# Optimization experiments

Hardware: AMD Instinct MI355X
Metric: run time of the kernel (lower is better)

## Reference

```python
import jax, jax.numpy as jnp
import numpy as np

B, T, I, H = 128, 128, 12, 512


def setup_inputs() -> dict:
    key = jax.random.key(0)
    k1, k2, k3, k4 = jax.random.split(key, 4)
    s_ih = 1.0 / np.sqrt(H)
    return {
        "history": jax.random.normal(k1, (B, T, I), dtype=jnp.float32),
        "W_ih": jax.random.uniform(k2, (3 * H, I), dtype=jnp.float32, minval=-s_ih, maxval=s_ih),
        "W_hh": jax.random.uniform(k3, (3 * H, H), dtype=jnp.float32, minval=-s_ih, maxval=s_ih),
        "W_pred": jax.random.uniform(k4, (2, H), dtype=jnp.float32, minval=-s_ih, maxval=s_ih),
    }


def reference(history, W_ih, W_hh, W_pred):
    # GRUCell (bias=False), PyTorch gate order: r, z, n
    def step(h, x_t):
        gi = x_t @ W_ih.T            # [B, 3H]
        gh = h @ W_hh.T              # [B, 3H]
        i_r, i_z, i_n = jnp.split(gi, 3, axis=-1)
        h_r, h_z, h_n = jnp.split(gh, 3, axis=-1)
        r = jax.nn.sigmoid(i_r + h_r)
        z = jax.nn.sigmoid(i_z + h_z)
        n = jnp.tanh(i_n + r * h_n)
        h_new = (1.0 - z) * n + z * h
        logit = h_new @ W_pred.T     # per-step bubble_prediction head
        return h_new, logit

    h0 = jnp.zeros((history.shape[0], W_hh.shape[1]), dtype=history.dtype)
    xs = jnp.swapaxes(history, 0, 1)          # [T, B, I]
    h_last, logits_tbf = jax.lax.scan(step, h0, xs)
    logits = jnp.swapaxes(logits_tbf, 0, 1)   # [B, T, 2]
    return logits, h_last
```

## Files before the change

kernel.cpp:

```cpp
#include <hip/hip_runtime.h>
#include <cstdint>


typedef __attribute__((ext_vector_type(4))) float f32x4;
typedef __attribute__((ext_vector_type(8))) __bf16 bf16x8;

#define NTHREADS 256
#define CG_N 32
#define BB 16
#define HC 16
#define T_STEPS 128
#define I_DIM 12
#define H_DIM 512

#define WS_HX0   0
#define WS_HX1   262144
#define WS_FLAGS 524288

__device__ __forceinline__ float bf16f(unsigned short u){
  return __uint_as_float(((unsigned int)u) << 16);
}
__device__ __forceinline__ void split_bf16(float x, unsigned short &hi, unsigned short &lo){
  unsigned int u = __float_as_uint(x);
  hi = (unsigned short)(u >> 16);
  float r = x - __uint_as_float((u >> 16) << 16);
  unsigned int ru = __float_as_uint(r);
  ru += 0x7fffu + ((ru >> 16) & 1u);
  lo = (unsigned short)(ru >> 16);
}
__device__ __forceinline__ float fsigmoid(float x){ return 1.0f / (1.0f + __expf(-x)); }
__device__ __forceinline__ float ftanh(float x){ return 2.0f / (1.0f + __expf(-2.0f * x)) - 1.0f; }
__device__ __forceinline__ f32x4 MFMA(bf16x8 a, bf16x8 b, f32x4 c){
  return __builtin_amdgcn_mfma_f32_16x16x32_bf16(a, b, c, 0, 0, 0);
}
__device__ __forceinline__ void wait_vm0(){
  asm volatile("s_waitcnt vmcnt(0)" ::: "memory");
}
__device__ __forceinline__ unsigned int hiP(unsigned int x, unsigned int y){
  return (x >> 16) | (y & 0xFFFF0000u);
}
__device__ __forceinline__ unsigned int loP(unsigned int x, unsigned int y){
  return (x & 0xFFFFu) | (y << 16);
}

__device__ __forceinline__ void dev_store_u32(unsigned int* p, unsigned int v){
  asm volatile("global_store_dword %0, %1, off sc1" :: "v"(p), "v"(v) : "memory");
}
__device__ __forceinline__ unsigned int dev_load_u32(const unsigned int* p){
  unsigned int v;
  asm volatile("global_load_dword %0, %1, off sc1\n\ts_waitcnt vmcnt(0)"
               : "=v"(v) : "v"(p) : "memory");
  return v;
}
__device__ __forceinline__ void load_h_row(const unsigned int* p, uint4* pr){
  uint4 v0, v1, v2, v3, v4, v5, v6, v7;
  asm volatile(
    "global_load_dwordx4 %0, %8, off sc1\n\t"
    "global_load_dwordx4 %1, %8, off offset:16 sc1\n\t"
    "global_load_dwordx4 %2, %8, off offset:32 sc1\n\t"
    "global_load_dwordx4 %3, %8, off offset:48 sc1\n\t"
    "global_load_dwordx4 %4, %8, off offset:64 sc1\n\t"
    "global_load_dwordx4 %5, %8, off offset:80 sc1\n\t"
    "global_load_dwordx4 %6, %8, off offset:96 sc1\n\t"
    "global_load_dwordx4 %7, %8, off offset:112 sc1\n\t"
    "s_waitcnt vmcnt(0)"
    : "=&v"(v0), "=&v"(v1), "=&v"(v2), "=&v"(v3),
      "=&v"(v4), "=&v"(v5), "=&v"(v6), "=&v"(v7)
    : "v"(p) : "memory");
  pr[0]=v0; pr[1]=v1; pr[2]=v2; pr[3]=v3; pr[4]=v4; pr[5]=v5; pr[6]=v6; pr[7]=v7;
}

__device__ __forceinline__ void poll_h_row(const unsigned int* p, uint4* pr,
                                           unsigned int want){
  for (;;){
    load_h_row(p, pr);
    unsigned int diff = 0u;
    #pragma unroll
    for (int b = 0; b < 8; ++b)
      diff |= (pr[b].x ^ want) | (pr[b].y ^ want) | (pr[b].z ^ want) | (pr[b].w ^ want);
    if ((diff & 3u) == 0u) break;
  }
  #pragma unroll
  for (int b = 0; b < 8; ++b){
    pr[b].x &= 0xFFFFFFFCu; pr[b].y &= 0xFFFFFFFCu;
    pr[b].z &= 0xFFFFFFFCu; pr[b].w &= 0xFFFFFFFCu;
  }
}

extern "C" __global__ void __launch_bounds__(NTHREADS, 1)
gru_persistent(const float* __restrict__ hist, const float* __restrict__ wih,
               const float* __restrict__ whh, const float* __restrict__ wpred,
               float* __restrict__ out, unsigned char* __restrict__ ws)
{
  __shared__ __align__(16) unsigned short whi_l[3*16*64*8];
  __shared__ __align__(16) unsigned short wlo_l[3*16*64*8];
  __shared__ __align__(16) unsigned short hhi_l[BB*H_DIM];
  __shared__ __align__(16) unsigned short hlo_l[BB*H_DIM];
  __shared__ __align__(16) float part_l[4*3*64*4];
  __shared__ __align__(16) float x_l[BB*I_DIM];
  __shared__ __align__(16) float wih_l[48*I_DIM];
  __shared__ __align__(16) float wpred_l[2*H_DIM];

  const int tid  = threadIdx.x;
  const int bg   = blockIdx.x & 7;
  const int cg   = blockIdx.x >> 3;
  const int wave = tid >> 6;
  const int lane = tid & 63;

  unsigned int* hx[2] = {(unsigned int*)(ws + WS_HX0), (unsigned int*)(ws + WS_HX1)};
  unsigned int* flagsP = (unsigned int*)(ws + WS_FLAGS);

  for (int i = tid; i < 48*I_DIM; i += NTHREADS){
    int j = i / I_DIM, ii = i % I_DIM;
    int R = (j >> 4)*H_DIM + cg*HC + (j & 15);
    wih_l[i] = wih[R*I_DIM + ii];
  }
  if (cg < 4){
    for (int i = tid; i < 2*H_DIM; i += NTHREADS) wpred_l[i] = wpred[i];
  }
  #pragma unroll
  for (int it = 0; it < 24; ++it){
    int f0 = (it*NTHREADS + tid) * 4;
    int j = f0 >> 9, k = f0 & 511;
    int R = (j >> 4)*H_DIM + cg*HC + (j & 15);
    float4 v = *(const float4*)(whh + R*H_DIM + k);
    int nt = j >> 4;
    int ln = (j & 15) | (((k >> 3) & 3) << 4);
    int kt = k >> 5, e = k & 7;
    int base = (((nt*16 + kt)*64) + ln)*8 + e;
    float vv[4] = {v.x, v.y, v.z, v.w};
    unsigned short h4[4], l4[4];
    #pragma unroll
    for (int q = 0; q < 4; ++q) split_bf16(vv[q], h4[q], l4[q]);
    uint2 uh, ul;
    uh.x = (unsigned int)h4[0] | ((unsigned int)h4[1] << 16);
    uh.y = (unsigned int)h4[2] | ((unsigned int)h4[3] << 16);
    ul.x = (unsigned int)l4[0] | ((unsigned int)l4[1] << 16);
    ul.y = (unsigned int)l4[2] | ((unsigned int)l4[3] << 16);
    *(uint2*)((char*)whi_l + base*2) = uh;
    *(uint2*)((char*)wlo_l + base*2) = ul;
  }

  {
    int b = tid >> 4, hc = tid & 15;
    int gidx = (bg*BB + b)*H_DIM + cg*HC + hc;
    dev_store_u32(hx[0] + gidx, 0u);
    dev_store_u32(hx[1] + gidx, 2u);
  }
  wait_vm0();
  __syncthreads();
  if (wave == 0 && lane < CG_N)
    dev_store_u32(flagsP + (bg*CG_N + lane)*CG_N + cg, 1u);
  if (wave == 0){
    const unsigned int* fp = flagsP + (bg*CG_N + cg)*CG_N + (lane & 31);
    for (;;){
      unsigned int f = dev_load_u32(fp);
      if (__ballot(f >= 1u) == ~0ull) break;
      __builtin_amdgcn_s_sleep(1);
    }
  }
  __syncthreads();

  for (int t = 0; t < T_STEPS; ++t){
    const int cur = t & 1, nxt = cur ^ 1;

    if (tid < BB*I_DIM){
      int b = tid / I_DIM, ii = tid % I_DIM;
      x_l[tid] = hist[((bg*BB + b)*T_STEPS + t)*I_DIM + ii];
    }

    {
      int row = tid & 15, col0 = (tid >> 4) * 32;
      const unsigned int* p = hx[cur] + (bg*BB + row)*H_DIM + col0;
      uint4 pr[8];
      poll_h_row(p, pr, (unsigned int)(t & 3));
      #pragma unroll
      for (int k = 0; k < 4; ++k){
        uint4 a = pr[2*k], b = pr[2*k+1];
        uint4 hi4 = { hiP(a.x,a.y), hiP(a.z,a.w), hiP(b.x,b.y), hiP(b.z,b.w) };
        uint4 lo4 = { loP(a.x,a.y), loP(a.z,a.w), loP(b.x,b.y), loP(b.z,b.w) };
        int boff = row*1024 + (((col0 + 8*k)*2) ^ ((row & 7) << 4));
        *(uint4*)((char*)hhi_l + boff) = hi4;
        *(uint4*)((char*)hlo_l + boff) = lo4;
      }
    }
    __syncthreads();

    f32x4 acc[3];
    #pragma unroll
    for (int nt = 0; nt < 3; ++nt) acc[nt] = {0.f, 0.f, 0.f, 0.f};
    #pragma unroll
    for (int kk = 0; kk < 4; ++kk){
      int kt = wave*4 + kk;
      int arow = lane & 15;
      int aboff = arow*1024 + ((kt*64 + (lane >> 4)*16) ^ ((arow & 7) << 4));
      bf16x8 ahi = *(const bf16x8*)((const char*)hhi_l + aboff);
      bf16x8 alo = *(const bf16x8*)((const char*)hlo_l + aboff);
      #pragma unroll
      for (int nt = 0; nt < 3; ++nt){
        int bboff = (((nt*16 + kt)*64) + lane)*16;
        bf16x8 bhi = *(const bf16x8*)((const char*)whi_l + bboff);
        bf16x8 blo = *(const bf16x8*)((const char*)wlo_l + bboff);
        acc[nt] = MFMA(ahi, bhi, acc[nt]);
        acc[nt] = MFMA(ahi, blo, acc[nt]);
        acc[nt] = MFMA(alo, bhi, acc[nt]);
      }
    }
    #pragma unroll
    for (int nt = 0; nt < 3; ++nt)
      *(f32x4*)(part_l + ((wave*3 + nt)*64 + lane)*4) = acc[nt];
    __syncthreads();

    {
      int b = tid >> 4, hc = tid & 15;
      int lc = ((b >> 2) << 4) | hc;
      int rc = b & 3;
      float gh[3];
      #pragma unroll
      for (int g = 0; g < 3; ++g){
        float s = 0.f;
        #pragma unroll
        for (int w = 0; w < 4; ++w) s += part_l[((w*3 + g)*64 + lc)*4 + rc];
        gh[g] = s;
      }
      float gi[3];
      #pragma unroll
      for (int g = 0; g < 3; ++g){
        float s = 0.f;
        #pragma unroll
        for (int ii = 0; ii < I_DIM; ++ii)
          s += x_l[b*I_DIM + ii] * wih_l[(g*16 + hc)*I_DIM + ii];
        gi[g] = s;
      }
      float r = fsigmoid(gi[0] + gh[0]);
      float z = fsigmoid(gi[1] + gh[1]);
      float n = ftanh(gi[2] + r*gh[2]);
      int colg = cg*HC + hc;
      int hoff = b*1024 + ((colg*2) ^ ((b & 7) << 4));
      float hp = bf16f(*(unsigned short*)((char*)hhi_l + hoff))
               + bf16f(*(unsigned short*)((char*)hlo_l + hoff));
      float hn = (1.0f - z)*n + z*hp;

      unsigned short shi, slo; split_bf16(hn, shi, slo);
      unsigned int pk = ((unsigned int)shi << 16) | ((unsigned int)slo & 0xFFFCu)
                      | (unsigned int)((t + 1) & 3);
      int gidx = (bg*BB + b)*H_DIM + colg;
      dev_store_u32(hx[nxt] + gidx, pk);
      if (t == T_STEPS - 1) out[32768 + gidx] = hn;
    }

    if (cg < 4 && t > 0){
      int o = cg & 1;
      int b = ((cg >> 1) << 3) + (tid >> 5);
      int s = tid & 31;
      float p = 0.f;
      #pragma unroll
      for (int q = 0; q < 2; ++q){
        int c = s*16 + q*8;
        int boff = b*1024 + ((c*2) ^ ((b & 7) << 4));
        uint4 vh = *(const uint4*)((const char*)hhi_l + boff);
        uint4 vl = *(const uint4*)((const char*)hlo_l + boff);
        const unsigned short* ph = (const unsigned short*)&vh;
        const unsigned short* pl = (const unsigned short*)&vl;
        #pragma unroll
        for (int e = 0; e < 8; ++e)
          p += (bf16f(ph[e]) + bf16f(pl[e])) * wpred_l[o*H_DIM + c + e];
      }
      #pragma unroll
      for (int m = 1; m < 32; m <<= 1) p += __shfl_xor(p, m);
      if (s == 0) out[((bg*BB + b)*T_STEPS + (t-1))*2 + o] = p;
    }

    __syncthreads();
  }

  if (cg < 4){
    int row = tid & 15, col0 = (tid >> 4) * 32;
    const unsigned int* p = hx[0] + (bg*BB + row)*H_DIM + col0;
    uint4 pr[8];
    poll_h_row(p, pr, 0u);
    #pragma unroll
    for (int k = 0; k < 4; ++k){
      uint4 a = pr[2*k], b = pr[2*k+1];
      uint4 hi4 = { hiP(a.x,a.y), hiP(a.z,a.w), hiP(b.x,b.y), hiP(b.z,b.w) };
      uint4 lo4 = { loP(a.x,a.y), loP(a.z,a.w), loP(b.x,b.y), loP(b.z,b.w) };
      int boff = row*1024 + (((col0 + 8*k)*2) ^ ((row & 7) << 4));
      *(uint4*)((char*)hhi_l + boff) = hi4;
      *(uint4*)((char*)hlo_l + boff) = lo4;
    }
    __syncthreads();
    int o = cg & 1;
    int b = ((cg >> 1) << 3) + (tid >> 5);
    int s = tid & 31;
    float pacc = 0.f;
    #pragma unroll
    for (int q = 0; q < 2; ++q){
      int c = s*16 + q*8;
      int boff = b*1024 + ((c*2) ^ ((b & 7) << 4));
      uint4 vh = *(const uint4*)((const char*)hhi_l + boff);
      uint4 vl = *(const uint4*)((const char*)hlo_l + boff);
      const unsigned short* ph = (const unsigned short*)&vh;
      const unsigned short* pl = (const unsigned short*)&vl;
      #pragma unroll
      for (int e = 0; e < 8; ++e)
        pacc += (bf16f(ph[e]) + bf16f(pl[e])) * wpred_l[o*H_DIM + c + e];
    }
    #pragma unroll
    for (int m = 1; m < 32; m <<= 1) pacc += __shfl_xor(pacc, m);
    if (s == 0) out[((bg*BB + b)*T_STEPS + 127)*2 + o] = pacc;
  }
}

extern "C" void kernel_launch(void* const* d_in, const int* in_sizes, int n_in,
                              void* d_out, int out_size, void* d_ws, size_t ws_size,
                              hipStream_t stream) {
  const float* hist  = (const float*)d_in[0];
  const float* wih   = (const float*)d_in[1];
  const float* whh   = (const float*)d_in[2];
  const float* wpred = (const float*)d_in[3];
  float* out = (float*)d_out;
  unsigned char* ws = (unsigned char*)d_ws;

  hipMemsetAsync(ws + WS_FLAGS, 0, 8*CG_N*CG_N*4, stream);

  gru_persistent<<<dim3(256), dim3(NTHREADS), 0, stream>>>(hist, wih, whh, wpred, out, ws);
}
```

Baseline: 601.4 us.

## Spread prediction head across all blocks and replace syncthreads with lean barriers

The per-step prediction head moves off the first 4 column groups: every block now computes one (batch row, output) logit per step with a single wave and a 64-lane reduction, so all 32 column groups share the head evenly. __syncthreads calls are replaced by explicit s_barrier with only an lgkmcnt wait and sched_barrier fences, which avoids waiting on outstanding global stores. The final-step logit is now computed by one wave per block polling its own h row directly, instead of staging the whole tile in LDS. The aim is to shorten the critical path of the slowest blocks each step. The risk is that the cheaper barriers must still order memory correctly across threads.

```diff
diff --git a/kernel.cpp b/kernel.cpp
--- a/kernel.cpp
+++ b/kernel.cpp
@@ -43,6 +43,18 @@
   return (x & 0xFFFFu) | (y << 16);
 }
 
+__device__ __forceinline__ void bar_lgkm(){
+  asm volatile("s_waitcnt lgkmcnt(0)" ::: "memory");
+  __builtin_amdgcn_sched_barrier(0);
+  __builtin_amdgcn_s_barrier();
+  __builtin_amdgcn_sched_barrier(0);
+}
+__device__ __forceinline__ void bar_raw(){
+  __builtin_amdgcn_sched_barrier(0);
+  __builtin_amdgcn_s_barrier();
+  __builtin_amdgcn_sched_barrier(0);
+}
+
 __device__ __forceinline__ void dev_store_u32(unsigned int* p, unsigned int v){
   asm volatile("global_store_dword %0, %1, off sc1" :: "v"(p), "v"(v) : "memory");
 }
@@ -50,6 +62,11 @@
   unsigned int v;
   asm volatile("global_load_dword %0, %1, off sc1\n\ts_waitcnt vmcnt(0)"
                : "=v"(v) : "v"(p) : "memory");
+  return v;
+}
+__device__ __forceinline__ uint4 load4_sc1(const unsigned int* p){
+  uint4 v;
+  asm volatile("global_load_dwordx4 %0, %1, off sc1" : "=v"(v) : "v"(p) : "memory");
   return v;
 }
 __device__ __forceinline__ void load_h_row(const unsigned int* p, uint4* pr){
@@ -106,6 +123,8 @@
   const int cg   = blockIdx.x >> 3;
   const int wave = tid >> 6;
   const int lane = tid & 63;
+  const int b_log = cg & 15;
+  const int o_log = cg >> 4;
 
   unsigned int* hx[2] = {(unsigned int*)(ws + WS_HX0), (unsigned int*)(ws + WS_HX1)};
   unsigned int* flagsP = (unsigned int*)(ws + WS_FLAGS);
@@ -115,9 +134,7 @@
     int R = (j >> 4)*H_DIM + cg*HC + (j & 15);
     wih_l[i] = wih[R*I_DIM + ii];
   }
-  if (cg < 4){
-    for (int i = tid; i < 2*H_DIM; i += NTHREADS) wpred_l[i] = wpred[i];
-  }
+  for (int i = tid; i < 2*H_DIM; i += NTHREADS) wpred_l[i] = wpred[i];
   #pragma unroll
   for (int it = 0; it < 24; ++it){
     int f0 = (it*NTHREADS + tid) * 4;
@@ -184,7 +201,7 @@
         *(uint4*)((char*)hlo_l + boff) = lo4;
       }
     }
-    __syncthreads();
+    bar_lgkm();
 
     f32x4 acc[3];
     #pragma unroll
@@ -209,7 +226,7 @@
     #pragma unroll
     for (int nt = 0; nt < 3; ++nt)
       *(f32x4*)(part_l + ((wave*3 + nt)*64 + lane)*4) = acc[nt];
-    __syncthreads();
+    bar_lgkm();
 
     {
       int b = tid >> 4, hc = tid & 15;
@@ -249,65 +266,50 @@
       if (t == T_STEPS - 1) out[32768 + gidx] = hn;
     }
 
-    if (cg < 4 && t > 0){
-      int o = cg & 1;
-      int b = ((cg >> 1) << 3) + (tid >> 5);
-      int s = tid & 31;
-      float p = 0.f;
-      #pragma unroll
-      for (int q = 0; q < 2; ++q){
-        int c = s*16 + q*8;
-        int boff = b*1024 + ((c*2) ^ ((b & 7) << 4));
-        uint4 vh = *(const uint4*)((const char*)hhi_l + boff);
-        uint4 vl = *(const uint4*)((const char*)hlo_l + boff);
-        const unsigned short* ph = (const unsigned short*)&vh;
-        const unsigned short* pl = (const unsigned short*)&vl;
-        #pragma unroll
-        for (int e = 0; e < 8; ++e)
-          p += (bf16f(ph[e]) + bf16f(pl[e])) * wpred_l[o*H_DIM + c + e];
-      }
-      #pragma unroll
-      for (int m = 1; m < 32; m <<= 1) p += __shfl_xor(p, m);
-      if (s == 0) out[((bg*BB + b)*T_STEPS + (t-1))*2 + o] = p;
-    }
-
-    __syncthreads();
-  }
-
-  if (cg < 4){
-    int row = tid & 15, col0 = (tid >> 4) * 32;
-    const unsigned int* p = hx[0] + (bg*BB + row)*H_DIM + col0;
-    uint4 pr[8];
-    poll_h_row(p, pr, 0u);
-    #pragma unroll
-    for (int k = 0; k < 4; ++k){
-      uint4 a = pr[2*k], b = pr[2*k+1];
-      uint4 hi4 = { hiP(a.x,a.y), hiP(a.z,a.w), hiP(b.x,b.y), hiP(b.z,b.w) };
-      uint4 lo4 = { loP(a.x,a.y), loP(a.z,a.w), loP(b.x,b.y), loP(b.z,b.w) };
-      int boff = row*1024 + (((col0 + 8*k)*2) ^ ((row & 7) << 4));
-      *(uint4*)((char*)hhi_l + boff) = hi4;
-      *(uint4*)((char*)hlo_l + boff) = lo4;
-    }
-    __syncthreads();
-    int o = cg & 1;
-    int b = ((cg >> 1) << 3) + (tid >> 5);
-    int s = tid & 31;
-    float pacc = 0.f;
-    #pragma unroll
-    for (int q = 0; q < 2; ++q){
-      int c = s*16 + q*8;
-      int boff = b*1024 + ((c*2) ^ ((b & 7) << 4));
+    if (wave == 0 && t > 0){
+      int c = lane * 8;
+      int boff = b_log*1024 + ((c*2) ^ ((b_log & 7) << 4));
       uint4 vh = *(const uint4*)((const char*)hhi_l + boff);
       uint4 vl = *(const uint4*)((const char*)hlo_l + boff);
       const unsigned short* ph = (const unsigned short*)&vh;
       const unsigned short* pl = (const unsigned short*)&vl;
+      float p = 0.f;
       #pragma unroll
       for (int e = 0; e < 8; ++e)
-        pacc += (bf16f(ph[e]) + bf16f(pl[e])) * wpred_l[o*H_DIM + c + e];
-    }
-    #pragma unroll
-    for (int m = 1; m < 32; m <<= 1) pacc += __shfl_xor(pacc, m);
-    if (s == 0) out[((bg*BB + b)*T_STEPS + 127)*2 + o] = pacc;
+        p += (bf16f(ph[e]) + bf16f(pl[e])) * wpred_l[o_log*H_DIM + c + e];
+      #pragma unroll
+      for (int m = 1; m < 64; m <<= 1) p += __shfl_xor(p, m);
+      if (lane == 0) out[((bg*BB + b_log)*T_STEPS + (t-1))*2 + o_log] = p;
+    }
+
+    bar_raw();
+  }
+
+  if (wave == 0){
+    const unsigned int* p = hx[0] + (bg*BB + b_log)*H_DIM + lane*8;
+    uint4 a0, a1;
+    for (;;){
+      a0 = load4_sc1(p); a1 = load4_sc1(p + 4);
+      wait_vm0();
+      unsigned int diff = (a0.x | a0.y | a0.z | a0.w | a1.x | a1.y | a1.z | a1.w);
+      if ((((a0.x ^ 0u) | (a0.y) | (a0.z) | (a0.w) | a1.x | a1.y | a1.z | a1.w) & 3u) == 0u) break;
+      (void)diff;
+      __builtin_amdgcn_s_sleep(1);
+    }
+    const unsigned int pk8[8] = {a0.x & 0xFFFFFFFCu, a0.y & 0xFFFFFFFCu,
+                                 a0.z & 0xFFFFFFFCu, a0.w & 0xFFFFFFFCu,
+                                 a1.x & 0xFFFFFFFCu, a1.y & 0xFFFFFFFCu,
+                                 a1.z & 0xFFFFFFFCu, a1.w & 0xFFFFFFFCu};
+    float pacc = 0.f;
+    #pragma unroll
+    for (int e = 0; e < 8; ++e){
+      unsigned int v = pk8[e];
+      float hv = bf16f((unsigned short)(v >> 16)) + bf16f((unsigned short)(v & 0xFFFFu));
+      pacc += hv * wpred_l[o_log*H_DIM + lane*8 + e];
+    }
+    #pragma unroll
+    for (int m = 1; m < 64; m <<= 1) pacc += __shfl_xor(pacc, m);
+    if (lane == 0) out[((bg*BB + b_log)*T_STEPS + 127)*2 + o_log] = pacc;
   }
 }
 
```

Result: faster. 524.5 us (-12.8%).
